# Optimization experiments

Measured on AMD Instinct MI355X. Metric: run time of the kernel, lower is better.

Reference implementation:

```python
import jax, jax.numpy as jnp
import numpy as np
from jax import lax

EPS = 1e-5  # BatchNorm / LayerNorm eps
B, DIM, H, W = 32, 256, 64, 64
S = 64            # state_dim
D_INNER = 256     # ssd_expand * dim
HIDDEN = 1024     # mlp_ratio * dim


def _bn(x, g, b, m, v):
    # BatchNorm2d, inference mode with given running stats. x: (B,C,H,W)
    inv = lax.rsqrt(v + EPS)
    return (x - m[None, :, None, None]) * (g * inv)[None, :, None, None] + b[None, :, None, None]


def _dwconv3x3(x, w):
    # depthwise 3x3 conv, stride 1, SAME padding. w: (C,1,3,3)
    return lax.conv_general_dilated(
        x, w, window_strides=(1, 1), padding='SAME',
        feature_group_count=x.shape[1],
        dimension_numbers=('NCHW', 'OIHW', 'NCHW'))


def setup_inputs() -> dict:
    key = jax.random.key(0)
    ks = jax.random.split(key, 32)
    n = lambda i, shp, s=0.02: jax.random.normal(ks[i], shp, jnp.float32) * s
    u = lambda i, shp: jax.random.uniform(ks[i], shp, jnp.float32)
    return {
        'x': jax.random.normal(ks[0], (B, DIM, H, W), jnp.float32),
        # dwconv1 (Conv2dNorm depthwise)
        'dw1_w': n(1, (DIM, 1, 3, 3)), 'dw1_g': 1.0 + n(2, (DIM,)), 'dw1_b': n(3, (DIM,)),
        'dw1_m': n(4, (DIM,)), 'dw1_v': u(5, (DIM,)) + 0.5,
        # LayerNorm1d
        'ln_w': 1.0 + n(6, (DIM,)), 'ln_b': n(7, (DIM,)),
        # mixer (HSMSSD)
        'bcdt_w': n(8, (3 * S, DIM)),
        'dwm_w': n(9, (3 * S, 1, 3, 3)),
        'A_param': 1.0 + 15.0 * u(10, (S,)),
        'hz_w': n(11, (2 * D_INNER, DIM)),
        'out_w': n(12, (DIM, D_INNER)),
        'D_param': jnp.ones((1,), jnp.float32),
        # dwconv2
        'dw2_w': n(13, (DIM, 1, 3, 3)), 'dw2_g': 1.0 + n(14, (DIM,)), 'dw2_b': n(15, (DIM,)),
        'dw2_m': n(16, (DIM,)), 'dw2_v': u(17, (DIM,)) + 0.5,
        # FFN
        'fc1_w': n(18, (HIDDEN, DIM)), 'fc1_g': 1.0 + n(19, (HIDDEN,)), 'fc1_b': n(20, (HIDDEN,)),
        'fc1_m': n(21, (HIDDEN,)), 'fc1_v': u(22, (HIDDEN,)) + 0.5,
        'fc2_w': n(23, (DIM, HIDDEN)), 'fc2_g': 1.0 + n(24, (DIM,)), 'fc2_b': n(25, (DIM,)),
        'fc2_m': n(26, (DIM,)), 'fc2_v': u(27, (DIM,)) + 0.5,
        # alpha-gated residual blends
        'alpha': 1e-4 * jnp.ones((4, DIM), jnp.float32) + n(28, (4, DIM), 0.01),
    }


def reference(x, dw1_w, dw1_g, dw1_b, dw1_m, dw1_v, ln_w, ln_b,
              bcdt_w, dwm_w, A_param, hz_w, out_w, D_param,
              dw2_w, dw2_g, dw2_b, dw2_m, dw2_v,
              fc1_w, fc1_g, fc1_b, fc1_m, fc1_v,
              fc2_w, fc2_g, fc2_b, fc2_m, fc2_v, alpha):
    b, dim, h_, w_ = x.shape
    L = h_ * w_
    a = jax.nn.sigmoid(alpha)[:, :, None, None]  # (4, dim, 1, 1)

    # alpha-blended depthwise conv 1
    x = (1.0 - a[0]) * x + a[0] * _bn(_dwconv3x3(x, dw1_w), dw1_g, dw1_b, dw1_m, dw1_v)
    x_prev = x

    # LayerNorm1d over channel dim on (B, C, L)
    xf = x.reshape(b, dim, L)
    mean = xf.mean(axis=1, keepdims=True)
    var = ((xf - mean) ** 2).mean(axis=1, keepdims=True)
    xn = (xf - mean) * lax.rsqrt(var + EPS) * ln_w[None, :, None] + ln_b[None, :, None]

    # HSMSSD mixer
    bc_dt = jnp.einsum('bcl,oc->bol', xn, bcdt_w).reshape(b, 3 * S, h_, w_)
    bc_dt = _dwconv3x3(bc_dt, dwm_w).reshape(b, 3 * S, L)
    Bm, Cm, dt = jnp.split(bc_dt, 3, axis=1)          # each (B, S, L)
    Am = jax.nn.softmax(dt + A_param[None, :, None], axis=-1)
    AB = Am * Bm                                      # (B, S, L)
    h = jnp.einsum('bcl,bsl->bcs', xn, AB)            # (B, dim, S)
    hz = jnp.einsum('bcs,oc->bos', h, hz_w)           # (B, 2*d_inner, S)
    hh, z = jnp.split(hz, 2, axis=1)
    hg = hh * jax.nn.silu(z) + hh * D_param[0]
    hout = jnp.einsum('bcs,oc->bos', hg, out_w)       # (B, dim, S)
    y = jnp.einsum('bcs,bsl->bcl', hout, Cm).reshape(b, dim, h_, w_)

    x = (1.0 - a[1]) * x_prev + a[1] * y
    x = (1.0 - a[2]) * x + a[2] * _bn(_dwconv3x3(x, dw2_w), dw2_g, dw2_b, dw2_m, dw2_v)

    # FFN: 1x1 conv + BN + ReLU + 1x1 conv + BN
    t = _bn(jnp.einsum('bchw,oc->bohw', x, fc1_w), fc1_g, fc1_b, fc1_m, fc1_v)
    t = jax.nn.relu(t)
    t = _bn(jnp.einsum('bchw,oc->bohw', t, fc2_w), fc2_g, fc2_b, fc2_m, fc2_v)
    x = (1.0 - a[3]) * x + a[3] * t
    return (x, hout)
```

## Files before the change

kernel.cpp:

```cpp
#include <hip/hip_runtime.h>
#include <hip/hip_bf16.h>

typedef __hip_bfloat16 bf16;
typedef __attribute__((ext_vector_type(8))) short bf16x8;
typedef __attribute__((ext_vector_type(4))) float f32x4;

__device__ __forceinline__ float LD(const float* p){ return *p; }
__device__ __forceinline__ float LD(const bf16* p){ return __bfloat162float(*p); }
__device__ __forceinline__ void ST(float* p, float v){ *p = v; }
__device__ __forceinline__ void ST(bf16* p, float v){ *p = __float2bfloat16(v); }
__device__ __forceinline__ float sigm(float v){ return 1.f/(1.f + expf(-v)); }
__device__ __forceinline__ ushort f2b(float f){
    unsigned u = __float_as_uint(f);
    return (ushort)((u + 0x7fffu + ((u>>16)&1u)) >> 16);
}

#define NEPS 1e-5f

template<typename TIN, typename TOUT>
__global__ __launch_bounds__(256) void dwconv_bn_blend(
        const TIN* __restrict__ xin, TOUT* __restrict__ xout,
        const float* __restrict__ w, const float* __restrict__ gg, const float* __restrict__ bb,
        const float* __restrict__ mm, const float* __restrict__ vv,
        const float* __restrict__ alpha, int arow)
{
    __shared__ float tile[66*66];
    int blk = blockIdx.x;
    int ch = blk & 255;
    const TIN* xp = xin + (size_t)blk*4096;
    TOUT* op = xout + (size_t)blk*4096;
    int tid = threadIdx.x;
    for (int i = tid; i < 66*66; i += 256) {
        int r = i/66, c = i%66;
        int gr = r-1, gc = c-1;
        float val = 0.f;
        if (gr >= 0 && gr < 64 && gc >= 0 && gc < 64) val = LD(&xp[gr*64+gc]);
        tile[i] = val;
    }
    __syncthreads();
    float wv[9];
    #pragma unroll
    for (int k=0;k<9;k++) wv[k] = w[ch*9+k];
    float sc = gg[ch] * rsqrtf(vv[ch] + NEPS);
    float mv = mm[ch], bv = bb[ch];
    float av = sigm(alpha[arow*256+ch]);
    for (int p = tid; p < 4096; p += 256) {
        int r = p>>6, c = p&63;
        float a = 0.f;
        #pragma unroll
        for (int dr=0;dr<3;dr++)
            #pragma unroll
            for (int dc=0;dc<3;dc++)
                a += wv[dr*3+dc]*tile[(r+dr)*66 + (c+dc)];
        float bn = (a - mv)*sc + bv;
        float xv = tile[(r+1)*66 + (c+1)];
        ST(&op[p], (1.f-av)*xv + av*bn);
    }
}

template<typename TX>
__global__ __launch_bounds__(256) void ln_stats(const TX* __restrict__ x1,
        float* __restrict__ meanp, float* __restrict__ invp)
{
    int blk = blockIdx.x;
    int b = blk >> 4;
    int l = ((blk & 15) << 8) + threadIdx.x;
    const TX* xp = x1 + (size_t)b*256*4096 + l;
    float mean = 0.f, m2 = 0.f;
    for (int c=0;c<256;c++){ float v = LD(&xp[(size_t)c*4096]); mean += v; m2 += v*v; }
    mean *= (1.f/256.f); m2 *= (1.f/256.f);
    meanp[b*4096 + l] = mean;
    invp[b*4096 + l] = rsqrtf(m2 - mean*mean + NEPS);
}

__global__ __launch_bounds__(256) void prep_k(
        const float* __restrict__ f1w, const float* __restrict__ f2w,
        const float* __restrict__ bcdtw,
        const float* __restrict__ g1, const float* __restrict__ b1,
        const float* __restrict__ m1, const float* __restrict__ v1,
        const float* __restrict__ g2, const float* __restrict__ b2,
        const float* __restrict__ m2, const float* __restrict__ v2,
        ushort* __restrict__ w1bf, ushort* __restrict__ w2bf,
        ushort* __restrict__ wbc,
        float* __restrict__ sc1, float* __restrict__ sb1,
        float* __restrict__ sc2, float* __restrict__ sb2)
{
    int i = blockIdx.x*256 + threadIdx.x;
    if (i < 262144) {
        w1bf[i] = f2b(f1w[i]);
        w2bf[i] = f2b(f2w[i]);
    }
    if (i < 49152) wbc[i] = f2b(bcdtw[i]);
    if (i < 1024) { float s = g1[i]*rsqrtf(v1[i]+NEPS); sc1[i]=s; sb1[i]=b1[i]-m1[i]*s; }
    if (i < 256)  { float s = g2[i]*rsqrtf(v2[i]+NEPS); sc2[i]=s; sb2[i]=b2[i]-m2[i]*s; }
}

template<typename TX>
__global__ __launch_bounds__(256) void bcdt_mfma(
        const TX* __restrict__ x1,
        const float* __restrict__ meanp, const float* __restrict__ invp,
        const float* __restrict__ lnw, const float* __restrict__ lnb,
        const ushort* __restrict__ wbc,
        bf16* __restrict__ bc, ushort* __restrict__ xn_bf, int b0)
{
    __shared__ __align__(16) ushort Xs[64*256];
    int blk = blockIdx.x;
    int lb = blk >> 6;
    int b  = b0 + lb;
    int l0 = (blk & 63) << 6;
    int tid = threadIdx.x, lane = tid & 63, w = tid >> 6;
    const TX* xp = x1 + (size_t)b*256*4096 + l0;
    float mval = meanp[b*4096 + l0 + lane];
    float ival = invp [b*4096 + l0 + lane];
    ushort* xnp = xn_bf + (size_t)lb*256*4096 + l0;

    for (int cc = w*8; cc < 256; cc += 32) {
        ushort u[8];
        #pragma unroll
        for (int j=0;j<8;j++){
            float v = LD(&xp[(size_t)(cc+j)*4096 + lane]);
            float xn = (v - mval)*ival*lnw[cc+j] + lnb[cc+j];
            u[j] = f2b(xn);
            xnp[(size_t)(cc+j)*4096 + lane] = u[j];
        }
        uint4 pk;
        pk.x = (uint)u[0] | ((uint)u[1]<<16);
        pk.y = (uint)u[2] | ((uint)u[3]<<16);
        pk.z = (uint)u[4] | ((uint)u[5]<<16);
        pk.w = (uint)u[6] | ((uint)u[7]<<16);
        int g = (cc>>3) ^ (lane&7);
        *(uint4*)&Xs[lane*256 + g*8] = pk;
    }
    __syncthreads();

    f32x4 zero4 = {0.f,0.f,0.f,0.f};
    f32x4 acc[3][4];
    #pragma unroll
    for (int m=0;m<3;m++)
        #pragma unroll
        for (int f=0;f<4;f++) acc[m][f] = zero4;

    int hbase = w*48;
    #pragma unroll
    for (int ks=0; ks<8; ks++){
        bf16x8 afr[3];
        #pragma unroll
        for (int m=0;m<3;m++)
            afr[m] = *(const bf16x8*)&wbc[(size_t)(hbase + m*16 + (lane&15))*256
                                          + ks*32 + (lane>>4)*8];
        #pragma unroll
        for (int f=0;f<4;f++){
            int px = f*16 + (lane&15);
            int g = (ks*4 + (lane>>4)) ^ (px&7);
            bf16x8 bfr = *(const bf16x8*)&Xs[px*256 + g*8];
            #pragma unroll
            for (int m=0;m<3;m++)
                acc[m][f] = __builtin_amdgcn_mfma_f32_16x16x32_bf16(afr[m], bfr, acc[m][f], 0,0,0);
        }
    }
    bf16* op = bc + (size_t)lb*192*4096 + l0;
    #pragma unroll
    for (int m=0;m<3;m++)
        #pragma unroll
        for (int r=0;r<4;r++){
            int o = hbase + m*16 + (lane>>4)*4 + r;
            #pragma unroll
            for (int f=0;f<4;f++){
                int px = f*16 + (lane&15);
                op[(size_t)o*4096 + px] = __float2bfloat16(acc[m][f][r]);
            }
        }
}

__global__ __launch_bounds__(256) void dwconv_plain(bf16* __restrict__ data, const float* __restrict__ w)
{
    __shared__ float tile[66*66];
    int blk = blockIdx.x;
    int ch = blk % 192;
    bf16* xp = data + (size_t)blk*4096;
    int tid = threadIdx.x;
    for (int i = tid; i < 66*66; i += 256) {
        int r = i/66, c = i%66;
        int gr = r-1, gc = c-1;
        float val = 0.f;
        if (gr >= 0 && gr < 64 && gc >= 0 && gc < 64) val = LD(&xp[gr*64+gc]);
        tile[i] = val;
    }
    __syncthreads();
    float wv[9];
    #pragma unroll
    for (int k=0;k<9;k++) wv[k] = w[ch*9+k];
    for (int p = tid; p < 4096; p += 256) {
        int r = p>>6, c = p&63;
        float a = 0.f;
        #pragma unroll
        for (int dr=0;dr<3;dr++)
            #pragma unroll
            for (int dc=0;dc<3;dc++)
                a += wv[dr*3+dc]*tile[(r+dr)*66 + (c+dc)];
        ST(&xp[p], a);
    }
}

__global__ __launch_bounds__(256) void softmax_ab(bf16* __restrict__ bc, const float* __restrict__ A)
{
    __shared__ float red[8];
    int blk = blockIdx.x;
    int lb = blk >> 6;
    int s = blk & 63;
    bf16* dtp = bc + ((size_t)lb*192 + 128 + s)*4096;
    bf16* bmp = bc + ((size_t)lb*192 + s)*4096;
    int tid = threadIdx.x;
    float Av = A[s];
    float vals[16];
    float mx = -1e30f;
    #pragma unroll
    for (int i=0;i<16;i++){ vals[i] = LD(&dtp[i*256+tid]) + Av; mx = fmaxf(mx, vals[i]); }
    #pragma unroll
    for (int o=32;o>0;o>>=1) mx = fmaxf(mx, __shfl_down(mx, o));
    int lane = tid & 63, wid = tid >> 6;
    if (lane == 0) red[wid] = mx;
    __syncthreads();
    if (tid == 0) red[4] = fmaxf(fmaxf(red[0],red[1]), fmaxf(red[2],red[3]));
    __syncthreads();
    mx = red[4];
    float sum = 0.f;
    #pragma unroll
    for (int i=0;i<16;i++){ vals[i] = expf(vals[i]-mx); sum += vals[i]; }
    #pragma unroll
    for (int o=32;o>0;o>>=1) sum += __shfl_down(sum, o);
    if (lane == 0) red[wid] = sum;
    __syncthreads();
    if (tid == 0) red[5] = red[0]+red[1]+red[2]+red[3];
    __syncthreads();
    float inv = 1.f/red[5];
    #pragma unroll
    for (int i=0;i<16;i++){
        float ab = vals[i]*inv*LD(&bmp[i*256+tid]);
        ST(&bmp[i*256+tid], ab);
    }
}

__global__ __launch_bounds__(256) void h_mfma(
        const ushort* __restrict__ xn_bf, const bf16* __restrict__ bc,
        float* __restrict__ h_part)
{
    int blk = blockIdx.x;
    int lb = blk >> 3;
    int kz = blk & 7;
    int kbase = kz*512;
    int tid = threadIdx.x, lane = tid & 63, w = tid >> 6;
    const ushort* ap = xn_bf + (size_t)lb*256*4096;
    const ushort* bp = (const ushort*)bc + (size_t)lb*192*4096;
    f32x4 zero4 = {0.f,0.f,0.f,0.f};
    f32x4 acc[4][4];
    #pragma unroll
    for (int m=0;m<4;m++)
        #pragma unroll
        for (int n=0;n<4;n++) acc[m][n] = zero4;

    for (int ks=0; ks<16; ks++){
        int koff = kbase + ks*32 + (lane>>4)*8;
        bf16x8 afr[4], bfr[4];
        #pragma unroll
        for (int m=0;m<4;m++)
            afr[m] = *(const bf16x8*)&ap[(size_t)(w*64 + m*16 + (lane&15))*4096 + koff];
        #pragma unroll
        for (int n=0;n<4;n++)
            bfr[n] = *(const bf16x8*)&bp[(size_t)(n*16 + (lane&15))*4096 + koff];
        #pragma unroll
        for (int m=0;m<4;m++)
            #pragma unroll
            for (int n=0;n<4;n++)
                acc[m][n] = __builtin_amdgcn_mfma_f32_16x16x32_bf16(afr[m], bfr[n], acc[m][n], 0,0,0);
    }
    float* hp = h_part + ((size_t)lb*8 + kz)*16384;
    #pragma unroll
    for (int m=0;m<4;m++)
        #pragma unroll
        for (int n=0;n<4;n++)
            #pragma unroll
            for (int r=0;r<4;r++){
                int c = w*64 + m*16 + (lane>>4)*4 + r;
                int s = n*16 + (lane&15);
                hp[c*64 + s] = acc[m][n][r];
            }
}

__global__ __launch_bounds__(256) void hz_gate(const float* __restrict__ h_part,
        const float* __restrict__ w, const float* __restrict__ Dp,
        float* __restrict__ hg)
{
    __shared__ float ht[256][64];
    int blk = blockIdx.x; int lb = blk>>2; int o0 = (blk&3)*64;
    int tid = threadIdx.x;
    const float* hp = h_part + (size_t)lb*8*16384;
    for (int i=tid;i<16384;i+=256){
        float s = 0.f;
        #pragma unroll
        for (int k=0;k<8;k++) s += hp[k*16384 + i];
        ht[i>>6][i&63] = s;
    }
    __syncthreads();
    int lane=tid&63, g=tid>>6;
    float Dv = Dp[0];
    for (int i4=0;i4<4;i4++){
        int ol = o0 + g*16 + i4*4;
        const float* r0 = w + (size_t)ol*256;
        const float *r1=r0+256, *r2=r0+512, *r3=r0+768;
        const float* z0 = w + (size_t)(ol+256)*256;
        const float *z1=z0+256, *z2=z0+512, *z3=z0+768;
        float d0=0.f,d1=0.f,d2=0.f,d3=0.f;
        float e0=0.f,e1=0.f,e2=0.f,e3=0.f;
        #pragma unroll 4
        for (int c4=0;c4<64;c4++){
            float x0=ht[c4*4][lane],x1v=ht[c4*4+1][lane],x2v=ht[c4*4+2][lane],x3v=ht[c4*4+3][lane];
            float4 a0=((const float4*)r0)[c4],a1=((const float4*)r1)[c4];
            float4 a2=((const float4*)r2)[c4],a3=((const float4*)r3)[c4];
            d0 += a0.x*x0+a0.y*x1v+a0.z*x2v+a0.w*x3v;
            d1 += a1.x*x0+a1.y*x1v+a1.z*x2v+a1.w*x3v;
            d2 += a2.x*x0+a2.y*x1v+a2.z*x2v+a2.w*x3v;
            d3 += a3.x*x0+a3.y*x1v+a3.z*x2v+a3.w*x3v;
            float4 b0=((const float4*)z0)[c4],b1=((const float4*)z1)[c4];
            float4 b2=((const float4*)z2)[c4],b3=((const float4*)z3)[c4];
            e0 += b0.x*x0+b0.y*x1v+b0.z*x2v+b0.w*x3v;
            e1 += b1.x*x0+b1.y*x1v+b1.z*x2v+b1.w*x3v;
            e2 += b2.x*x0+b2.y*x1v+b2.z*x2v+b2.w*x3v;
            e3 += b3.x*x0+b3.y*x1v+b3.z*x2v+b3.w*x3v;
        }
        float s0 = e0/(1.f+expf(-e0)) + Dv;
        float s1 = e1/(1.f+expf(-e1)) + Dv;
        float s2 = e2/(1.f+expf(-e2)) + Dv;
        float s3 = e3/(1.f+expf(-e3)) + Dv;
        size_t base = ((size_t)lb*256 + ol)*64 + lane;
        hg[base]=d0*s0; hg[base+64]=d1*s1; hg[base+128]=d2*s2; hg[base+192]=d3*s3;
    }
}

__global__ __launch_bounds__(256) void out_gemm(const float* __restrict__ hg, const float* __restrict__ w,
        ushort* __restrict__ hout_bf, float* __restrict__ hout_out, int b0)
{
    __shared__ float ht[256][64];
    int blk = blockIdx.x; int lb = blk>>2; int b = b0 + lb; int o0 = (blk&3)*64;
    int tid = threadIdx.x;
    const float* hp = hg + (size_t)lb*16384;
    for (int i=tid;i<16384;i+=256) ht[i>>6][i&63]=hp[i];
    __syncthreads();
    int lane=tid&63, g=tid>>6;
    for (int i4=0;i4<4;i4++){
        int ol = g*16 + i4*4;
        const float* r0 = w + (size_t)(o0+ol)*256;
        const float *r1=r0+256, *r2=r0+512, *r3=r0+768;
        float d0=0.f,d1=0.f,d2=0.f,d3=0.f;
        #pragma unroll 8
        for (int c4=0;c4<64;c4++){
            float x0=ht[c4*4][lane],x1v=ht[c4*4+1][lane],x2v=ht[c4*4+2][lane],x3v=ht[c4*4+3][lane];
            float4 a0=((const float4*)r0)[c4],a1=((const float4*)r1)[c4];
            float4 a2=((const float4*)r2)[c4],a3=((const float4*)r3)[c4];
            d0 += a0.x*x0+a0.y*x1v+a0.z*x2v+a0.w*x3v;
            d1 += a1.x*x0+a1.y*x1v+a1.z*x2v+a1.w*x3v;
            d2 += a2.x*x0+a2.y*x1v+a2.z*x2v+a2.w*x3v;
            d3 += a3.x*x0+a3.y*x1v+a3.z*x2v+a3.w*x3v;
        }
        size_t lbase = ((size_t)lb*256 + o0 + ol)*64 + lane;
        hout_bf[lbase]=f2b(d0); hout_bf[lbase+64]=f2b(d1);
        hout_bf[lbase+128]=f2b(d2); hout_bf[lbase+192]=f2b(d3);
        size_t gbase = ((size_t)b*256 + o0 + ol)*64 + lane;
        hout_out[gbase]=d0; hout_out[gbase+64]=d1;
        hout_out[gbase+128]=d2; hout_out[gbase+192]=d3;
    }
}

template<typename TX>
__global__ __launch_bounds__(256) void y_mfma(
        const ushort* __restrict__ hout_bf, const bf16* __restrict__ bc,
        TX* __restrict__ x1, const float* __restrict__ alpha, int b0)
{
    __shared__ __align__(16) ushort Cs[64*64];
    int blk = blockIdx.x; int lb = blk>>6; int b = b0 + lb; int l0 = (blk&63)<<6;
    int tid = threadIdx.x, lane = tid&63, w = tid>>6;
    const ushort* cp = (const ushort*)bc + ((size_t)lb*192 + 64)*4096 + l0;
    for (int sc = w*8; sc < 64; sc += 32){
        ushort u[8];
        #pragma unroll
        for (int j=0;j<8;j++) u[j] = cp[(size_t)(sc+j)*4096 + lane];
        uint4 pk;
        pk.x = (uint)u[0] | ((uint)u[1]<<16);
        pk.y = (uint)u[2] | ((uint)u[3]<<16);
        pk.z = (uint)u[4] | ((uint)u[5]<<16);
        pk.w = (uint)u[6] | ((uint)u[7]<<16);
        int g = (sc>>3) ^ (lane&7);
        *(uint4*)&Cs[lane*64 + g*8] = pk;
    }
    __syncthreads();

    f32x4 zero4 = {0.f,0.f,0.f,0.f};
    f32x4 acc[4][4];
    #pragma unroll
    for (int m=0;m<4;m++)
        #pragma unroll
        for (int f=0;f<4;f++) acc[m][f] = zero4;

    const ushort* ap = hout_bf + (size_t)lb*256*64;
    #pragma unroll
    for (int ks=0; ks<2; ks++){
        bf16x8 afr[4];
        #pragma unroll
        for (int m=0;m<4;m++)
            afr[m] = *(const bf16x8*)&ap[(size_t)(w*64 + m*16 + (lane&15))*64
                                          + ks*32 + (lane>>4)*8];
        #pragma unroll
        for (int f=0;f<4;f++){
            int px = f*16 + (lane&15);
            int s8 = ks*32 + (lane>>4)*8;
            int g = (s8>>3) ^ (px&7);
            bf16x8 bfr = *(const bf16x8*)&Cs[px*64 + g*8];
            #pragma unroll
            for (int m=0;m<4;m++)
                acc[m][f] = __builtin_amdgcn_mfma_f32_16x16x32_bf16(afr[m], bfr, acc[m][f], 0,0,0);
        }
    }

    TX* xpo = x1 + (size_t)b*256*4096 + l0;
    #pragma unroll
    for (int m=0;m<4;m++)
        #pragma unroll
        for (int r=0;r<4;r++){
            int c = w*64 + m*16 + (lane>>4)*4 + r;
            float av = sigm(alpha[256+c]);
            #pragma unroll
            for (int f=0;f<4;f++){
                int px = f*16 + (lane&15);
                float xv = LD(&xpo[(size_t)c*4096 + px]);
                ST(&xpo[(size_t)c*4096 + px], (1.f-av)*xv + av*acc[m][f][r]);
            }
        }
}

template<typename TX>
__global__ __launch_bounds__(256) void ffn_mfma(
        const TX* __restrict__ x,
        const ushort* __restrict__ w1bf,
        const ushort* __restrict__ w2bf,
        const float* __restrict__ sc1, const float* __restrict__ sb1,
        const float* __restrict__ sc2, const float* __restrict__ sb2,
        const float* __restrict__ alpha,
        float* __restrict__ out)
{
    __shared__ __align__(16) ushort Xs[64*256];
    __shared__ __align__(16) ushort Ts[64*128];
    int blk = blockIdx.x;
    int b = blk >> 6, l0 = (blk & 63) << 6;
    int tid = threadIdx.x, lane = tid & 63, w = tid >> 6;
    const TX* xp = x + (size_t)b*256*4096 + l0;

    for (int cc = w*8; cc < 256; cc += 32) {
        float v[8];
        #pragma unroll
        for (int j=0;j<8;j++) v[j] = LD(&xp[(size_t)(cc+j)*4096 + lane]);
        uint4 pk;
        pk.x = (uint)f2b(v[0]) | ((uint)f2b(v[1])<<16);
        pk.y = (uint)f2b(v[2]) | ((uint)f2b(v[3])<<16);
        pk.z = (uint)f2b(v[4]) | ((uint)f2b(v[5])<<16);
        pk.w = (uint)f2b(v[6]) | ((uint)f2b(v[7])<<16);
        int g = (cc>>3) ^ (lane&7);
        *(uint4*)&Xs[lane*256 + g*8] = pk;
    }
    __syncthreads();

    f32x4 zero4 = {0.f,0.f,0.f,0.f};
    f32x4 acc2[4][4];
    #pragma unroll
    for (int m=0;m<4;m++)
        #pragma unroll
        for (int f=0;f<4;f++) acc2[m][f] = zero4;

    for (int hc = 0; hc < 1024; hc += 128) {
        int hbase = hc + w*32;
        f32x4 c1[2][4];
        #pragma unroll
        for (int m=0;m<2;m++)
            #pragma unroll
            for (int f=0;f<4;f++) c1[m][f] = zero4;
        for (int ks = 0; ks < 8; ks++) {
            bf16x8 afr[2];
            #pragma unroll
            for (int m=0;m<2;m++)
                afr[m] = *(const bf16x8*)&w1bf[(size_t)(hbase + m*16 + (lane&15))*256
                                               + ks*32 + (lane>>4)*8];
            #pragma unroll
            for (int f=0;f<4;f++){
                int px = f*16 + (lane&15);
                int g = (ks*4 + (lane>>4)) ^ (px&7);
                bf16x8 bfr = *(const bf16x8*)&Xs[px*256 + g*8];
                #pragma unroll
                for (int m=0;m<2;m++)
                    c1[m][f] = __builtin_amdgcn_mfma_f32_16x16x32_bf16(afr[m], bfr, c1[m][f], 0,0,0);
            }
        }
        __syncthreads();
        #pragma unroll
        for (int m=0;m<2;m++){
            #pragma unroll
            for (int r=0;r<4;r++){
                int h = hbase + m*16 + (lane>>4)*4 + r;
                float s1 = sc1[h], bb1 = sb1[h];
                int hl = h - hc;
                #pragma unroll
                for (int f=0;f<4;f++){
                    int px = f*16 + (lane&15);
                    float t = fmaxf(c1[m][f][r]*s1 + bb1, 0.f);
                    int g = (hl>>3) ^ (px&7);
                    Ts[px*128 + g*8 + (hl&7)] = f2b(t);
                }
            }
        }
        __syncthreads();
        int c0 = w*64;
        for (int ks = 0; ks < 4; ks++) {
            bf16x8 afr[4];
            #pragma unroll
            for (int m=0;m<4;m++)
                afr[m] = *(const bf16x8*)&w2bf[(size_t)(c0 + m*16 + (lane&15))*1024
                                               + hc + ks*32 + (lane>>4)*8];
            #pragma unroll
            for (int f=0;f<4;f++){
                int px = f*16 + (lane&15);
                int hl = ks*32 + (lane>>4)*8;
                int g = (hl>>3) ^ (px&7);
                bf16x8 bfr = *(const bf16x8*)&Ts[px*128 + g*8];
                #pragma unroll
                for (int m=0;m<4;m++)
                    acc2[m][f] = __builtin_amdgcn_mfma_f32_16x16x32_bf16(afr[m], bfr, acc2[m][f], 0,0,0);
            }
        }
    }

    float* op = out + (size_t)b*256*4096 + l0;
    int c0 = w*64;
    #pragma unroll
    for (int m=0;m<4;m++){
        #pragma unroll
        for (int r=0;r<4;r++){
            int c = c0 + m*16 + (lane>>4)*4 + r;
            float a = sigm(alpha[768+c]);
            float s2 = sc2[c], bb2 = sb2[c];
            #pragma unroll
            for (int f=0;f<4;f++){
                int px = f*16 + (lane&15);
                float t2 = acc2[m][f][r]*s2 + bb2;
                float xv = LD(&xp[(size_t)c*4096 + px]);
                op[(size_t)c*4096 + px] = (1.f-a)*xv + a*t2;
            }
        }
    }
}

template<typename TX>
static void run_all(const float* x, TX* x1, float* d_out_x, float* hout_out,
                    const float* dw1w, const float* dw1g, const float* dw1b,
                    const float* dw1m, const float* dw1v,
                    const float* lnw, const float* lnb,
                    const ushort* wbc, const float* dwmw, const float* Ap,
                    const float* hzw, const float* outw, const float* Dp,
                    const float* dw2w, const float* dw2g, const float* dw2b,
                    const float* dw2m, const float* dw2v,
                    const ushort* w1bf, const ushort* w2bf,
                    const float* sc1, const float* sb1,
                    const float* sc2, const float* sb2,
                    const float* alpha,
                    float* meanp, float* invp, char* cbase, int NB,
                    hipStream_t stream)
{
    bf16*   bc      = (bf16*)cbase;
    ushort* xn_bf   = (ushort*)(cbase + (size_t)NB*1572864);
    float*  h_part  = (float*)(cbase + (size_t)NB*(1572864 + 2097152));
    float*  hg      = (float*)((char*)h_part + (size_t)NB*524288);
    ushort* hout_bf = (ushort*)((char*)hg + (size_t)NB*65536);

    dwconv_bn_blend<float,TX><<<8192,256,0,stream>>>(x, x1, dw1w,dw1g,dw1b,dw1m,dw1v, alpha, 0);
    ln_stats<TX><<<512,256,0,stream>>>(x1, meanp, invp);

    for (int b0 = 0; b0 < 32; b0 += NB) {
        bcdt_mfma<TX><<<NB*64,256,0,stream>>>(x1, meanp, invp, lnw, lnb, wbc, bc, xn_bf, b0);
        dwconv_plain<<<NB*192,256,0,stream>>>(bc, dwmw);
        softmax_ab<<<NB*64,256,0,stream>>>(bc, Ap);
        h_mfma<<<NB*8,256,0,stream>>>(xn_bf, bc, h_part);
        hz_gate<<<NB*4,256,0,stream>>>(h_part, hzw, Dp, hg);
        out_gemm<<<NB*4,256,0,stream>>>(hg, outw, hout_bf, hout_out, b0);
        y_mfma<TX><<<NB*64,256,0,stream>>>(hout_bf, bc, x1, alpha, b0);
    }

    dwconv_bn_blend<TX,TX><<<8192,256,0,stream>>>(x1, x1, dw2w,dw2g,dw2b,dw2m,dw2v, alpha, 2);
    ffn_mfma<TX><<<2048,256,0,stream>>>(x1, w1bf, w2bf, sc1, sb1, sc2, sb2, alpha, d_out_x);
}

extern "C" void kernel_launch(void* const* d_in, const int* in_sizes, int n_in,
                              void* d_out, int out_size, void* d_ws, size_t ws_size,
                              hipStream_t stream)
{
    (void)in_sizes; (void)n_in; (void)out_size;
    const float* x     = (const float*)d_in[0];
    const float* dw1w  = (const float*)d_in[1];
    const float* dw1g  = (const float*)d_in[2];
    const float* dw1b  = (const float*)d_in[3];
    const float* dw1m  = (const float*)d_in[4];
    const float* dw1v  = (const float*)d_in[5];
    const float* lnw   = (const float*)d_in[6];
    const float* lnb   = (const float*)d_in[7];
    const float* bcdtw = (const float*)d_in[8];
    const float* dwmw  = (const float*)d_in[9];
    const float* Ap    = (const float*)d_in[10];
    const float* hzw   = (const float*)d_in[11];
    const float* outw  = (const float*)d_in[12];
    const float* Dp    = (const float*)d_in[13];
    const float* dw2w  = (const float*)d_in[14];
    const float* dw2g  = (const float*)d_in[15];
    const float* dw2b  = (const float*)d_in[16];
    const float* dw2m  = (const float*)d_in[17];
    const float* dw2v  = (const float*)d_in[18];
    const float* f1w   = (const float*)d_in[19];
    const float* f1g   = (const float*)d_in[20];
    const float* f1b   = (const float*)d_in[21];
    const float* f1m   = (const float*)d_in[22];
    const float* f1v   = (const float*)d_in[23];
    const float* f2w   = (const float*)d_in[24];
    const float* f2g   = (const float*)d_in[25];
    const float* f2b_  = (const float*)d_in[26];
    const float* f2m   = (const float*)d_in[27];
    const float* f2v   = (const float*)d_in[28];
    const float* alpha = (const float*)d_in[29];

    const size_t nx = (size_t)32*256*4096;
    float* d_out_x  = (float*)d_out;
    float* hout_out = d_out_x + nx;

    char* ws = (char*)d_ws;
    float* meanp = (float*)ws;
    float* invp  = meanp + 131072;
    size_t off = 1048576;
    ushort* w1bf = (ushort*)(ws + off); off += 524288;
    ushort* w2bf = (ushort*)(ws + off); off += 524288;
    ushort* wbc  = (ushort*)(ws + off); off += 98304;
    float* sc1 = (float*)(ws + off); off += 4096;
    float* sb1 = (float*)(ws + off); off += 4096;
    float* sc2 = (float*)(ws + off); off += 1024;
    float* sb2 = (float*)(ws + off); off += 1024;
    off = (off + 255) & ~(size_t)255;

    const size_t perb = 1572864 + 2097152 + 524288 + 65536 + 32768;
    size_t avail = ws_size > off ? ws_size - off : 0;

    prep_k<<<1024,256,0,stream>>>(f1w, f2w, bcdtw, f1g,f1b,f1m,f1v, f2g,f2b_,f2m,f2v,
                                  w1bf, w2bf, wbc, sc1, sb1, sc2, sb2);

    if (avail >= nx*2 + 8*perb) {
        bf16* x1b = (bf16*)(ws + off); off += nx*2;
        char* cbase = ws + off;
        size_t a2 = ws_size - off;
        int NB = 8;
        for (int nb = 32; nb >= 8; nb >>= 1) if (a2 >= (size_t)nb*perb) { NB = nb; break; }
        run_all<bf16>(x, x1b, d_out_x, hout_out,
                      dw1w,dw1g,dw1b,dw1m,dw1v, lnw,lnb, wbc, dwmw, Ap, hzw, outw, Dp,
                      dw2w,dw2g,dw2b,dw2m,dw2v, w1bf,w2bf, sc1,sb1,sc2,sb2, alpha,
                      meanp, invp, cbase, NB, stream);
    } else {
        char* cbase = ws + off;
        int NB = 1;
        for (int nb = 32; nb >= 1; nb >>= 1) if (avail >= (size_t)nb*perb) { NB = nb; break; }
        run_all<float>(x, d_out_x, d_out_x, hout_out,
                       dw1w,dw1g,dw1b,dw1m,dw1v, lnw,lnb, wbc, dwmw, Ap, hzw, outw, Dp,
                       dw2w,dw2g,dw2b,dw2m,dw2v, w1bf,w2bf, sc1,sb1,sc2,sb2, alpha,
                       meanp, invp, cbase, NB, stream);
    }
}
```

Before: 689.5 us.

## Repartition FFN kernel per-wave over pixels to drop block barriers

Result: slower. 1.423 ms (+106.3%).

```diff
diff --git a/kernel.cpp b/kernel.cpp
--- a/kernel.cpp
+++ b/kernel.cpp
@@ -438,7 +438,7 @@
 }
 
 template<typename TX>
-__global__ __launch_bounds__(256) void ffn_mfma(
+__global__ __launch_bounds__(256) void ffn_nb(
         const TX* __restrict__ x,
         const ushort* __restrict__ w1bf,
         const ushort* __restrict__ w2bf,
@@ -448,10 +448,12 @@
         float* __restrict__ out)
 {
     __shared__ __align__(16) ushort Xs[64*256];
-    __shared__ __align__(16) ushort Ts[64*128];
+    __shared__ __align__(16) ushort Ts[4*16*64];
     int blk = blockIdx.x;
     int b = blk >> 6, l0 = (blk & 63) << 6;
     int tid = threadIdx.x, lane = tid & 63, w = tid >> 6;
+    int q = lane >> 4, lp = lane & 15;
+    int pxg = w*16 + lp;
     const TX* xp = x + (size_t)b*256*4096 + l0;
 
     for (int cc = w*8; cc < 256; cc += 32) {
@@ -469,89 +471,66 @@
     __syncthreads();
 
     f32x4 zero4 = {0.f,0.f,0.f,0.f};
-    f32x4 acc2[4][4];
-    #pragma unroll
-    for (int m=0;m<4;m++)
-        #pragma unroll
-        for (int f=0;f<4;f++) acc2[m][f] = zero4;
-
-    for (int hc = 0; hc < 1024; hc += 128) {
-        int hbase = hc + w*32;
-        f32x4 c1[2][4];
-        #pragma unroll
-        for (int m=0;m<2;m++)
-            #pragma unroll
-            for (int f=0;f<4;f++) c1[m][f] = zero4;
-        for (int ks = 0; ks < 8; ks++) {
-            bf16x8 afr[2];
-            #pragma unroll
-            for (int m=0;m<2;m++)
-                afr[m] = *(const bf16x8*)&w1bf[(size_t)(hbase + m*16 + (lane&15))*256
-                                               + ks*32 + (lane>>4)*8];
-            #pragma unroll
-            for (int f=0;f<4;f++){
-                int px = f*16 + (lane&15);
-                int g = (ks*4 + (lane>>4)) ^ (px&7);
-                bf16x8 bfr = *(const bf16x8*)&Xs[px*256 + g*8];
-                #pragma unroll
-                for (int m=0;m<2;m++)
-                    c1[m][f] = __builtin_amdgcn_mfma_f32_16x16x32_bf16(afr[m], bfr, c1[m][f], 0,0,0);
+    f32x4 acc2[16];
+    #pragma unroll
+    for (int m=0;m<16;m++) acc2[m] = zero4;
+
+    char* tsw = (char*)&Ts[w*1024];
+    int xrow = pxg*256, xsw = pxg&7;
+
+    for (int hc = 0; hc < 16; ++hc) {
+        f32x4 c1[4];
+        #pragma unroll
+        for (int m=0;m<4;m++) c1[m] = zero4;
+        #pragma unroll
+        for (int ks=0; ks<8; ks++){
+            bf16x8 bfr = *(const bf16x8*)&Xs[xrow + (((ks*4+q)^xsw)<<3)];
+            #pragma unroll
+            for (int m=0;m<4;m++){
+                bf16x8 afr = *(const bf16x8*)&w1bf[(size_t)(hc*64 + m*16 + lp)*256
+                                                   + ks*32 + q*8];
+                c1[m] = __builtin_amdgcn_mfma_f32_16x16x32_bf16(afr, bfr, c1[m], 0,0,0);
             }
         }
-        __syncthreads();
-        #pragma unroll
-        for (int m=0;m<2;m++){
-            #pragma unroll
-            for (int r=0;r<4;r++){
-                int h = hbase + m*16 + (lane>>4)*4 + r;
-                float s1 = sc1[h], bb1 = sb1[h];
-                int hl = h - hc;
-                #pragma unroll
-                for (int f=0;f<4;f++){
-                    int px = f*16 + (lane&15);
-                    float t = fmaxf(c1[m][f][r]*s1 + bb1, 0.f);
-                    int g = (hl>>3) ^ (px&7);
-                    Ts[px*128 + g*8 + (hl&7)] = f2b(t);
-                }
+        #pragma unroll
+        for (int m=0;m<4;m++){
+            int hl = m*16 + q*4;
+            int hg2 = hc*64 + hl;
+            float s0=sc1[hg2],s1=sc1[hg2+1],s2v=sc1[hg2+2],s3=sc1[hg2+3];
+            float q0=sb1[hg2],q1=sb1[hg2+1],q2v=sb1[hg2+2],q3=sb1[hg2+3];
+            float t0 = fmaxf(c1[m][0]*s0 + q0, 0.f);
+            float t1 = fmaxf(c1[m][1]*s1 + q1, 0.f);
+            float t2 = fmaxf(c1[m][2]*s2v + q2v, 0.f);
+            float t3 = fmaxf(c1[m][3]*s3 + q3, 0.f);
+            uint2 pk;
+            pk.x = (uint)f2b(t0) | ((uint)f2b(t1)<<16);
+            pk.y = (uint)f2b(t2) | ((uint)f2b(t3)<<16);
+            int slot = hl>>3, rem = (hl&7)<<1;
+            *(uint2*)(tsw + lp*128 + ((slot ^ (lp&7))<<4) + rem) = pk;
+        }
+        #pragma unroll
+        for (int ks2=0; ks2<2; ks2++){
+            int sr = ks2*4 + q;
+            bf16x8 bfr = *(const bf16x8*)(tsw + lp*128 + ((sr ^ (lp&7))<<4));
+            #pragma unroll
+            for (int m=0;m<16;m++){
+                bf16x8 afr = *(const bf16x8*)&w2bf[(size_t)(m*16 + lp)*1024
+                                                   + hc*64 + sr*8];
+                acc2[m] = __builtin_amdgcn_mfma_f32_16x16x32_bf16(afr, bfr, acc2[m], 0,0,0);
             }
         }
-        __syncthreads();
-        int c0 = w*64;
-        for (int ks = 0; ks < 4; ks++) {
-            bf16x8 afr[4];
-            #pragma unroll
-            for (int m=0;m<4;m++)
-                afr[m] = *(const bf16x8*)&w2bf[(size_t)(c0 + m*16 + (lane&15))*1024
-                                               + hc + ks*32 + (lane>>4)*8];
-            #pragma unroll
-            for (int f=0;f<4;f++){
-                int px = f*16 + (lane&15);
-                int hl = ks*32 + (lane>>4)*8;
-                int g = (hl>>3) ^ (px&7);
-                bf16x8 bfr = *(const bf16x8*)&Ts[px*128 + g*8];
-                #pragma unroll
-                for (int m=0;m<4;m++)
-                    acc2[m][f] = __builtin_amdgcn_mfma_f32_16x16x32_bf16(afr[m], bfr, acc2[m][f], 0,0,0);
-            }
-        }
     }
 
     float* op = out + (size_t)b*256*4096 + l0;
-    int c0 = w*64;
-    #pragma unroll
-    for (int m=0;m<4;m++){
+    #pragma unroll
+    for (int m=0;m<16;m++){
         #pragma unroll
         for (int r=0;r<4;r++){
-            int c = c0 + m*16 + (lane>>4)*4 + r;
+            int c = m*16 + q*4 + r;
             float a = sigm(alpha[768+c]);
-            float s2 = sc2[c], bb2 = sb2[c];
-            #pragma unroll
-            for (int f=0;f<4;f++){
-                int px = f*16 + (lane&15);
-                float t2 = acc2[m][f][r]*s2 + bb2;
-                float xv = LD(&xp[(size_t)c*4096 + px]);
-                op[(size_t)c*4096 + px] = (1.f-a)*xv + a*t2;
-            }
+            float t2 = acc2[m][r]*sc2[c] + sb2[c];
+            float xv = LD(&xp[(size_t)c*4096 + pxg]);
+            op[(size_t)c*4096 + pxg] = (1.f-a)*xv + a*t2;
         }
     }
 }
@@ -592,7 +571,7 @@
     }
 
     dwconv_bn_blend<TX,TX><<<8192,256,0,stream>>>(x1, x1, dw2w,dw2g,dw2b,dw2m,dw2v, alpha, 2);
-    ffn_mfma<TX><<<2048,256,0,stream>>>(x1, w1bf, w2bf, sc1, sb1, sc2, sb2, alpha, d_out_x);
+    ffn_nb<TX><<<2048,256,0,stream>>>(x1, w1bf, w2bf, sc1, sb1, sc2, sb2, alpha, d_out_x);
 }
 
 extern "C" void kernel_launch(void* const* d_in, const int* in_sizes, int n_in,
```
